# Kernel tuning notes

Measured on AMD Instinct MI355X. Metric: run time of the kernel, lower is better.

The kernel has to match this reference:

```python
import jax, jax.numpy as jnp
import numpy as np

B, C, N = 4, 512, 4096
CQK = C // 8


def setup_inputs() -> dict:
    key = jax.random.key(0)
    ks = jax.random.split(key, 8)
    return {
        "minibatch": jax.random.normal(ks[0], (B, C, N), dtype=jnp.float32),
        "Wq": jax.random.normal(ks[1], (CQK, C), dtype=jnp.float32) * 0.02,
        "bq": jax.random.normal(ks[2], (CQK,), dtype=jnp.float32) * 0.02,
        "Wk": jax.random.normal(ks[3], (CQK, C), dtype=jnp.float32) * 0.02,
        "bk": jax.random.normal(ks[4], (CQK,), dtype=jnp.float32) * 0.02,
        "Wv": jax.random.normal(ks[5], (C, C), dtype=jnp.float32) * 0.02,
        "bv": jax.random.normal(ks[6], (C,), dtype=jnp.float32) * 0.02,
        "gamma": jax.random.normal(ks[7], (1,), dtype=jnp.float32),
    }


def reference(minibatch, Wq, bq, Wk, bk, Wv, bv, gamma):
    # 1x1 Conv1d == per-position channel matmul. minibatch: [B, C, N]
    q = jnp.einsum('dc,bcn->bdn', Wq, minibatch) + bq[None, :, None]  # [B, C/8, N]
    k = jnp.einsum('dc,bcn->bdn', Wk, minibatch) + bk[None, :, None]  # [B, C/8, N]
    v = jnp.einsum('dc,bcn->bdn', Wv, minibatch) + bv[None, :, None]  # [B, C, N]
    # logits[b,i,j] = q_i . k_j  (note: original computes a triu mask but never uses it)
    logits = jnp.einsum('bdn,bdm->bnm', q, k)  # [B, N, N]
    probs = jax.nn.softmax(logits, axis=-1)
    # read[b,c,i] = sum_j v[b,c,j] * probs[b,i,j]
    read = jnp.einsum('bcm,bnm->bcn', v, probs)  # [B, C, N]
    return gamma[0] * read + minibatch
```

## Files before the change

### kernel.cpp

```cpp
#include <hip/hip_runtime.h>
#include <stdint.h>

typedef unsigned short u16;
typedef unsigned int u32;
typedef __attribute__((ext_vector_type(8))) short short8;
typedef __attribute__((ext_vector_type(4))) short s16x4;
typedef __attribute__((ext_vector_type(4))) float f32x4;
typedef __attribute__((ext_vector_type(16))) float f32x16;
typedef __attribute__((ext_vector_type(4))) int int4v;

#define MFMA16(a,b,c) __builtin_amdgcn_mfma_f32_16x16x32_bf16(a,b,c,0,0,0)
#define MFMA32(a,b,c) __builtin_amdgcn_mfma_f32_32x32x16_bf16(a,b,c,0,0,0)

constexpr int B_ = 4, C_ = 512, N_ = 4096, D_ = 64;

static __device__ __forceinline__ u16 f2bf(float f) {
    uint32_t u = __builtin_bit_cast(uint32_t, f);
    uint32_t r = (u + 0x7FFFu + ((u >> 16) & 1u)) >> 16;
    return (u16)r;
}

static __device__ __forceinline__ void gload_lds16(const void* g, void* l) {
    __builtin_amdgcn_global_load_lds(
        (const __attribute__((address_space(1))) u32*)g,
        (__attribute__((address_space(3))) u32*)l, 16, 0, 0);
}

__global__ void prep_w(const float* Wq, const float* bq, const float* Wk, const float* bk,
                       const float* Wv, const float* bv, u16* Wcat, float* biascat) {
    const float LOG2E = 1.44269504088896340736f;
    int idx = blockIdx.x * 256 + threadIdx.x;
    if (idx < 640 * 512) {
        int row = idx >> 9, col = idx & 511;
        float w;
        if (row < 64)        w = Wq[row * 512 + col] * LOG2E;
        else if (row < 128)  w = Wk[(row - 64) * 512 + col];
        else                 w = Wv[(row - 128) * 512 + col];
        Wcat[idx] = f2bf(w);
    }
    if (idx < 640) {
        float bb;
        if (idx < 64)        bb = bq[idx] * LOG2E;
        else if (idx < 128)  bb = bk[idx - 64];
        else                 bb = bv[idx - 128];
        biascat[idx] = bb;
    }
}

__global__ __launch_bounds__(256) void transpose_x(const float* __restrict__ x, u16* __restrict__ xT) {
    __shared__ float tile[64][65];
    int n0 = blockIdx.x * 64, c0 = blockIdx.y * 64, b = blockIdx.z;
    int t = threadIdx.x;
    int colq = (t & 15) * 4, rowb = t >> 4;
    const float* xb = x + (size_t)b * C_ * N_;
#pragma unroll
    for (int k = 0; k < 4; k++) {
        int row = rowb + 16 * k;
        float4 xv = *reinterpret_cast<const float4*>(&xb[(size_t)(c0 + row) * N_ + n0 + colq]);
        tile[row][colq + 0] = xv.x;
        tile[row][colq + 1] = xv.y;
        tile[row][colq + 2] = xv.z;
        tile[row][colq + 3] = xv.w;
    }
    __syncthreads();
    u16* xTb = xT + (size_t)b * N_ * C_;
#pragma unroll
    for (int k = 0; k < 4; k++) {
        int n = rowb + 16 * k;
        ushort4 o;
        o.x = f2bf(tile[colq + 0][n]);
        o.y = f2bf(tile[colq + 1][n]);
        o.z = f2bf(tile[colq + 2][n]);
        o.w = f2bf(tile[colq + 3][n]);
        *reinterpret_cast<ushort4*>(&xTb[(size_t)(n0 + n) * C_ + c0 + colq]) = o;
    }
}

__global__ __launch_bounds__(256) void proj_gemm(const u16* __restrict__ Wcat,
                                                 const float* __restrict__ biascat,
                                                 const u16* __restrict__ xT,
                                                 u16* __restrict__ qT, u16* __restrict__ kT,
                                                 u16* __restrict__ v) {
    int wg = blockIdx.x;
    int xcd = wg & 7, slot = wg >> 3;
    int b = xcd >> 1;
    int m0 = (slot >> 3) * 64;
    int n0 = ((xcd & 1) * 8 + (slot & 7)) * 256;
    int wave = threadIdx.x >> 6, lane = threadIdx.x & 63;
    n0 += wave * 64;
    int lr = lane & 15, lc = lane >> 4;
    const u16* xTb = xT + (size_t)b * N_ * C_;

    f32x4 acc[4][4] = {};
    short8 aF[4], bF[4], aFn[4], bFn[4];
#pragma unroll
    for (int ma = 0; ma < 4; ma++)
        aF[ma] = *reinterpret_cast<const short8*>(&Wcat[(size_t)(m0 + ma * 16 + lr) * 512 + lc * 8]);
#pragma unroll
    for (int na = 0; na < 4; na++)
        bF[na] = *reinterpret_cast<const short8*>(&xTb[(size_t)(n0 + na * 16 + lr) * 512 + lc * 8]);

    for (int k0 = 0; k0 < 512; k0 += 32) {
        if (k0 < 480) {
            int kn = k0 + 32;
#pragma unroll
            for (int ma = 0; ma < 4; ma++)
                aFn[ma] = *reinterpret_cast<const short8*>(&Wcat[(size_t)(m0 + ma * 16 + lr) * 512 + kn + lc * 8]);
#pragma unroll
            for (int na = 0; na < 4; na++)
                bFn[na] = *reinterpret_cast<const short8*>(&xTb[(size_t)(n0 + na * 16 + lr) * 512 + kn + lc * 8]);
        }
#pragma unroll
        for (int ma = 0; ma < 4; ma++)
#pragma unroll
            for (int na = 0; na < 4; na++)
                acc[ma][na] = MFMA16(aF[ma], bF[na], acc[ma][na]);
#pragma unroll
        for (int t = 0; t < 4; t++) { aF[t] = aFn[t]; bF[t] = bFn[t]; }
    }
#pragma unroll
    for (int ma = 0; ma < 4; ma++) {
#pragma unroll
        for (int r = 0; r < 4; r++) {
            int m = m0 + ma * 16 + lc * 4 + r;
            float bias = biascat[m];
#pragma unroll
            for (int na = 0; na < 4; na++) {
                int n = n0 + na * 16 + lr;
                u16 hv = f2bf(acc[ma][na][r] + bias);
                if (m < 64)
                    qT[((size_t)b * N_ + n) * D_ + m] = hv;
                else if (m < 128)
                    kT[((size_t)b * N_ + n) * D_ + (m - 64)] = hv;
                else {
                    int nl = n & 15;
                    int np = (nl & 3) | ((nl & 4) << 1) | ((nl & 8) >> 1);
                    v[((size_t)b * C_ + (m - 128)) * (size_t)N_ + (n & ~15) + np] = hv;
                }
            }
        }
    }
}

__global__ __launch_bounds__(512, 2) void attn(const u16* __restrict__ qT, const u16* __restrict__ kT,
                                               const u16* __restrict__ v, const float* __restrict__ x,
                                               const float* __restrict__ gamma_p, float* __restrict__ out) {
    int blk = blockIdx.x;
    int xcd = blk & 7, rest = blk >> 3;
    int b = xcd >> 1;
    int cs = (xcd & 1) + 2 * (rest & 1);
    int itile = rest >> 1;
    int c0 = cs * 128;
    int ib0 = itile * 256;

    int tid = threadIdx.x;
    int wv = tid >> 6, lane = tid & 63;
    int li = lane & 31, hi = lane >> 5;

    __shared__ char smem[98304];

    const u16* qTb = qT + (size_t)b * N_ * D_;
    const u16* kTb = kT + (size_t)b * N_ * D_;
    const u16* vb  = v  + (size_t)b * C_ * N_;

    short8 qf[4];
#pragma unroll
    for (int dc = 0; dc < 4; dc++)
        qf[dc] = *reinterpret_cast<const short8*>(
            &qTb[(size_t)(ib0 + wv * 32 + li) * D_ + dc * 16 + hi * 8]);

    f32x16 acc[4] = {};
    float lsum = 0.f;

    auto STAGE = [&](int t, int buf) {
        int jb = t * 128;
        char* Kb = smem + buf * 49152;
        char* Vb = Kb + 16384;
#pragma unroll
        for (int q = 0; q < 2; q++) {
            int ki = 2 * wv + q;
            int p = ki >> 1, jh2 = ki & 1;
            gload_lds16(kTb + (size_t)(jb + jh2 * 64 + lane) * D_ + p * 8,
                        Kb + p * 2048 + jh2 * 1024);
        }
#pragma unroll
        for (int q = 0; q < 4; q++) {
            int vi = 4 * wv + q;
            int qp = vi >> 1, ch = vi & 1;
            int j16b = qp >> 1, hb = qp & 1;
            gload_lds16(vb + (size_t)(c0 + ch * 64 + lane) * N_ + jb + j16b * 16 + hb * 8,
                        Vb + qp * 2048 + ch * 1024);
        }
    };

    STAGE(0, 0);
    asm volatile("s_waitcnt vmcnt(0)" ::: "memory");
    __builtin_amdgcn_s_barrier();
    asm volatile("" ::: "memory");

    for (int t = 0; t < 32; t++) {
        int buf = t & 1;
        char* Kb = smem + buf * 49152;
        char* Vb = Kb + 16384;

        if (t < 31) STAGE(t + 1, buf ^ 1);

#pragma unroll
        for (int jc = 0; jc < 4; jc++) {
            short8 kf0 = *reinterpret_cast<const short8*>(Kb + (0 + hi) * 2048 + (jc * 32 + li) * 16);
            short8 kf1 = *reinterpret_cast<const short8*>(Kb + (2 + hi) * 2048 + (jc * 32 + li) * 16);
            short8 kf2 = *reinterpret_cast<const short8*>(Kb + (4 + hi) * 2048 + (jc * 32 + li) * 16);
            short8 kf3 = *reinterpret_cast<const short8*>(Kb + (6 + hi) * 2048 + (jc * 32 + li) * 16);
            f32x16 S = {};
            S = MFMA32(kf0, qf[0], S);
            S = MFMA32(kf1, qf[1], S);
            S = MFMA32(kf2, qf[2], S);
            S = MFMA32(kf3, qf[3], S);
            float p[16];
#pragma unroll
            for (int r = 0; r < 16; r++) p[r] = __builtin_amdgcn_exp2f(S[r]);
            lsum += (((p[0]+p[1])+(p[2]+p[3]))+((p[4]+p[5])+(p[6]+p[7])))
                  + (((p[8]+p[9])+(p[10]+p[11]))+((p[12]+p[13])+(p[14]+p[15])));
            u32 w[8];
#pragma unroll
            for (int k = 0; k < 8; k++)
                asm("v_cvt_pk_bf16_f32 %0, %1, %2" : "=v"(w[k]) : "v"(p[2 * k]), "v"(p[2 * k + 1]));
            int4v a0 = { (int)w[0], (int)w[1], (int)w[2], (int)w[3] };
            int4v a1 = { (int)w[4], (int)w[5], (int)w[6], (int)w[7] };
            short8 PA0 = __builtin_bit_cast(short8, a0);
            short8 PA1 = __builtin_bit_cast(short8, a1);
#pragma unroll
            for (int ct = 0; ct < 4; ct++) {
                short8 vf0 = *reinterpret_cast<const short8*>(
                    Vb + ((jc * 2 + 0) * 2 + hi) * 2048 + (ct * 32 + li) * 16);
                short8 vf1 = *reinterpret_cast<const short8*>(
                    Vb + ((jc * 2 + 1) * 2 + hi) * 2048 + (ct * 32 + li) * 16);
                acc[ct] = MFMA32(PA0, vf0, acc[ct]);
                acc[ct] = MFMA32(PA1, vf1, acc[ct]);
            }
        }

        asm volatile("s_waitcnt vmcnt(0)" ::: "memory");
        __builtin_amdgcn_s_barrier();
        asm volatile("" ::: "memory");
    }

    float lfull = lsum + __shfl_xor(lsum, 32);
    float g = gamma_p[0];
    float* olds = reinterpret_cast<float*>(smem + wv * 4608);
    const float* xb = x + (size_t)b * C_ * N_;
    float* ob = out + (size_t)b * C_ * N_;
#pragma unroll
    for (int ct = 0; ct < 4; ct++) {
#pragma unroll
        for (int r = 0; r < 16; r++) {
            int crow = (r & 3) + 8 * (r >> 2) + 4 * hi;
            float linv = 1.0f / __shfl(lfull, crow);
            olds[li * 36 + crow] = g * acc[ct][r] * linv;
        }
        asm volatile("s_waitcnt lgkmcnt(0)" ::: "memory");
#pragma unroll
        for (int cp = 0; cp < 4; cp++) {
            int c_l = cp * 8 + (lane >> 3);
            int i4 = (lane & 7) * 4;
            float4 o4 = *reinterpret_cast<const float4*>(&olds[c_l * 36 + i4]);
            size_t off = (size_t)(c0 + ct * 32 + c_l) * N_ + ib0 + wv * 32 + i4;
            float4 xv = *reinterpret_cast<const float4*>(&xb[off]);
            float4 ov = { o4.x + xv.x, o4.y + xv.y, o4.z + xv.z, o4.w + xv.w };
            *reinterpret_cast<float4*>(&ob[off]) = ov;
        }
        asm volatile("s_waitcnt lgkmcnt(0)" ::: "memory");
    }
}

extern "C" void kernel_launch(void* const* d_in, const int* in_sizes, int n_in,
                              void* d_out, int out_size, void* d_ws, size_t ws_size,
                              hipStream_t stream) {
    const float* x     = (const float*)d_in[0];
    const float* Wq    = (const float*)d_in[1];
    const float* bq    = (const float*)d_in[2];
    const float* Wk    = (const float*)d_in[3];
    const float* bk    = (const float*)d_in[4];
    const float* Wv    = (const float*)d_in[5];
    const float* bv    = (const float*)d_in[6];
    const float* gamma = (const float*)d_in[7];
    float* out = (float*)d_out;

    char* ws = (char*)d_ws;
    u16*   xT      = (u16*)ws;
    u16*   Wcat    = (u16*)(ws + (size_t)16777216);
    float* biascat = (float*)(ws + (size_t)16777216 + 655360);
    u16*   qT      = (u16*)(ws + (size_t)16777216 + 655360 + 4096);
    u16*   kT      = qT + (size_t)B_ * N_ * D_;
    u16*   v       = kT + (size_t)B_ * N_ * D_;

    prep_w<<<1280, 256, 0, stream>>>(Wq, bq, Wk, bk, Wv, bv, Wcat, biascat);
    transpose_x<<<dim3(N_ / 64, C_ / 64, B_), 256, 0, stream>>>(x, xT);
    proj_gemm<<<640, 256, 0, stream>>>(Wcat, biascat, xT, qT, kT, v);
    attn<<<256, 512, 0, stream>>>(qT, kT, v, x, gamma, out);
}
```

Before: 173.4 us.

## Merge weight prep into transpose kernel and software-pipeline S/PV phases in attention

```diff
diff --git a/kernel.cpp b/kernel.cpp
--- a/kernel.cpp
+++ b/kernel.cpp
@@ -26,28 +26,32 @@
         (__attribute__((address_space(3))) u32*)l, 16, 0, 0);
 }
 
-__global__ void prep_w(const float* Wq, const float* bq, const float* Wk, const float* bk,
-                       const float* Wv, const float* bv, u16* Wcat, float* biascat) {
+__global__ __launch_bounds__(256) void prep_and_transpose(
+        const float* __restrict__ x, u16* __restrict__ xT,
+        const float* __restrict__ Wq, const float* __restrict__ bq,
+        const float* __restrict__ Wk, const float* __restrict__ bk,
+        const float* __restrict__ Wv, const float* __restrict__ bv,
+        u16* __restrict__ Wcat, float* __restrict__ biascat) {
     const float LOG2E = 1.44269504088896340736f;
-    int idx = blockIdx.x * 256 + threadIdx.x;
-    if (idx < 640 * 512) {
-        int row = idx >> 9, col = idx & 511;
-        float w;
-        if (row < 64)        w = Wq[row * 512 + col] * LOG2E;
-        else if (row < 128)  w = Wk[(row - 64) * 512 + col];
-        else                 w = Wv[(row - 128) * 512 + col];
-        Wcat[idx] = f2bf(w);
-    }
-    if (idx < 640) {
-        float bb;
-        if (idx < 64)        bb = bq[idx] * LOG2E;
-        else if (idx < 128)  bb = bk[idx - 64];
-        else                 bb = bv[idx - 128];
-        biascat[idx] = bb;
-    }
-}
-
-__global__ __launch_bounds__(256) void transpose_x(const float* __restrict__ x, u16* __restrict__ xT) {
+    if (blockIdx.z == B_) {
+        int base = (blockIdx.y * 64 + blockIdx.x) * 256 + threadIdx.x;
+        for (int idx = base; idx < 640 * 512; idx += 64 * 8 * 256) {
+            int row = idx >> 9, col = idx & 511;
+            float w;
+            if (row < 64)        w = Wq[row * 512 + col] * LOG2E;
+            else if (row < 128)  w = Wk[(row - 64) * 512 + col];
+            else                 w = Wv[(row - 128) * 512 + col];
+            Wcat[idx] = f2bf(w);
+        }
+        if (base < 640) {
+            float bb;
+            if (base < 64)       bb = bq[base] * LOG2E;
+            else if (base < 128) bb = bk[base - 64];
+            else                 bb = bv[base - 128];
+            biascat[base] = bb;
+        }
+        return;
+    }
     __shared__ float tile[64][65];
     int n0 = blockIdx.x * 64, c0 = blockIdx.y * 64, b = blockIdx.z;
     int t = threadIdx.x;
@@ -205,8 +209,7 @@
 
         if (t < 31) STAGE(t + 1, buf ^ 1);
 
-#pragma unroll
-        for (int jc = 0; jc < 4; jc++) {
+        auto S_PHASE = [&](int jc, short8* PAo) {
             short8 kf0 = *reinterpret_cast<const short8*>(Kb + (0 + hi) * 2048 + (jc * 32 + li) * 16);
             short8 kf1 = *reinterpret_cast<const short8*>(Kb + (2 + hi) * 2048 + (jc * 32 + li) * 16);
             short8 kf2 = *reinterpret_cast<const short8*>(Kb + (4 + hi) * 2048 + (jc * 32 + li) * 16);
@@ -227,18 +230,30 @@
                 asm("v_cvt_pk_bf16_f32 %0, %1, %2" : "=v"(w[k]) : "v"(p[2 * k]), "v"(p[2 * k + 1]));
             int4v a0 = { (int)w[0], (int)w[1], (int)w[2], (int)w[3] };
             int4v a1 = { (int)w[4], (int)w[5], (int)w[6], (int)w[7] };
-            short8 PA0 = __builtin_bit_cast(short8, a0);
-            short8 PA1 = __builtin_bit_cast(short8, a1);
+            PAo[0] = __builtin_bit_cast(short8, a0);
+            PAo[1] = __builtin_bit_cast(short8, a1);
+        };
+        auto PV_PHASE = [&](int jc, const short8* PAi) {
 #pragma unroll
             for (int ct = 0; ct < 4; ct++) {
                 short8 vf0 = *reinterpret_cast<const short8*>(
                     Vb + ((jc * 2 + 0) * 2 + hi) * 2048 + (ct * 32 + li) * 16);
                 short8 vf1 = *reinterpret_cast<const short8*>(
                     Vb + ((jc * 2 + 1) * 2 + hi) * 2048 + (ct * 32 + li) * 16);
-                acc[ct] = MFMA32(PA0, vf0, acc[ct]);
-                acc[ct] = MFMA32(PA1, vf1, acc[ct]);
+                acc[ct] = MFMA32(PAi[0], vf0, acc[ct]);
+                acc[ct] = MFMA32(PAi[1], vf1, acc[ct]);
             }
-        }
+        };
+
+        short8 PA_A[2], PA_B[2];
+        S_PHASE(0, PA_A);
+        S_PHASE(1, PA_B);
+        PV_PHASE(0, PA_A);
+        S_PHASE(2, PA_A);
+        PV_PHASE(1, PA_B);
+        S_PHASE(3, PA_B);
+        PV_PHASE(2, PA_A);
+        PV_PHASE(3, PA_B);
 
         asm volatile("s_waitcnt vmcnt(0)" ::: "memory");
         __builtin_amdgcn_s_barrier();
@@ -294,8 +309,8 @@
     u16*   kT      = qT + (size_t)B_ * N_ * D_;
     u16*   v       = kT + (size_t)B_ * N_ * D_;
 
-    prep_w<<<1280, 256, 0, stream>>>(Wq, bq, Wk, bk, Wv, bv, Wcat, biascat);
-    transpose_x<<<dim3(N_ / 64, C_ / 64, B_), 256, 0, stream>>>(x, xT);
+    prep_and_transpose<<<dim3(N_ / 64, C_ / 64, B_ + 1), 256, 0, stream>>>(
+        x, xT, Wq, bq, Wk, bk, Wv, bv, Wcat, biascat);
     proj_gemm<<<640, 256, 0, stream>>>(Wcat, biascat, xT, qT, kT, v);
     attn<<<256, 512, 0, stream>>>(qT, kT, v, x, gamma, out);
 }
```

Result: faster. 169.1 us (-2.4%).
